# Kernel optimization log

Hardware: AMD Instinct MI355X
Metric: run time of the kernel (lower is better)

Reference implementation:

```python
import jax, jax.numpy as jnp
import numpy as np

# --- model hyperparams (match PointFeatureNet / FastFlow3D SetConvLayer) ---
B, N, IN_CH = 4, 4096, 6
K = 64                      # max_num_neighbors in radius query (PyG FlowNet3D convention)
R1, RATIO1 = 0.5, 0.5       # set_conv_1
R2, RATIO2 = 1.0, 0.25      # set_conv_2
MLP1_DIMS = [IN_CH, 32, 32, 64]        # concat(feat(3), dpos(3)) -> 64
MLP2_DIMS = [64 + 3, 64, 64, 128]      # concat(feat(64), dpos(3)) -> 128


def _mlp_params(key, dims, scale=0.1):
    params = []
    for cin, cout in zip(dims[:-1], dims[1:]):
        key, kw, kb = jax.random.split(key, 3)
        params.append((jax.random.normal(kw, (cin, cout), jnp.float32) * scale,
                       jax.random.normal(kb, (cout,), jnp.float32) * scale))
    return params, key


def setup_inputs() -> dict:
    key = jax.random.key(0)
    key, kx = jax.random.split(key)
    x = jax.random.normal(kx, (B, N, IN_CH), jnp.float32)
    p1, key = _mlp_params(key, MLP1_DIMS)
    p2, key = _mlp_params(key, MLP2_DIMS)
    (w1a, b1a), (w1b, b1b), (w1c, b1c) = p1
    (w2a, b2a), (w2b, b2b), (w2c, b2c) = p2
    return {"x": x,
            "w1a": w1a, "b1a": b1a, "w1b": w1b, "b1b": b1b, "w1c": w1c, "b1c": b1c,
            "w2a": w2a, "b2a": b2a, "w2b": w2b, "b2b": b2b, "w2c": w2c, "b2c": b2c}


def fps(pos, n_samples):
    """Farthest point sampling on one cloud. pos: [N,3] -> idx [n_samples] int32.
    Deterministic start at index 0 (PyG fps uses a random start)."""
    n = pos.shape[0]
    def step(carry, _):
        min_d, last = carry
        d = jnp.sum((pos - pos[last]) ** 2, axis=-1)
        min_d = jnp.minimum(min_d, d)
        nxt = jnp.argmax(min_d).astype(jnp.int32)
        return (min_d, nxt), nxt
    init = (jnp.full((n,), jnp.inf, pos.dtype), jnp.asarray(0, jnp.int32))
    _, idx = jax.lax.scan(step, init, None, length=n_samples - 1)
    return jnp.concatenate([jnp.zeros((1,), jnp.int32), idx])


def ball_query(pos, q_pos, r):
    """Fixed-size radius query: up to K lowest-index points within r of each query.
    pos: [N,3], q_pos: [S,3] -> (idx [S,K] int32, valid [S,K] bool)."""
    n = pos.shape[0]
    d2 = jnp.sum((q_pos[:, None, :] - pos[None, :, :]) ** 2, axis=-1)   # [S,N]
    in_r = d2 <= (r * r)
    # prefer lowest source index among in-radius points (mimics PyG radius ordering)
    score = jnp.where(in_r, -jnp.arange(n, dtype=jnp.float32), -jnp.inf)
    s, idx = jax.lax.top_k(score, K)
    valid = jnp.isfinite(s)
    idx = jnp.where(valid, idx, 0).astype(jnp.int32)
    return idx, valid


def set_conv(feat, pos, r, ratio, params):
    """SetConvLayer: fps -> radius grouping -> PointNetConv(local MLP) -> max-pool.
    feat: [B,N,C], pos: [B,N,3] -> (feat' [B,S,Cout], pos' [B,S,3])."""
    n = pos.shape[1]
    s = int(n * ratio)
    idx = jax.vmap(lambda p: fps(p, s))(pos)                              # [B,S]
    q_pos = jax.vmap(lambda p, i: p[i])(pos, idx)                         # [B,S,3]
    nidx, valid = jax.vmap(lambda p, q: ball_query(p, q, r))(pos, q_pos)  # [B,S,K]
    npos = jax.vmap(lambda p, i: p[i])(pos, nidx)                         # [B,S,K,3]
    nfeat = jax.vmap(lambda f, i: f[i])(feat, nidx)                       # [B,S,K,C]
    # PointNetConv message: concat(x_j, pos_j - pos_i) -> MLP (Linear+ReLU chain)
    h = jnp.concatenate([nfeat, npos - q_pos[:, :, None, :]], axis=-1)    # [B,S,K,C+3]
    for w, b in params:
        h = jax.nn.relu(h @ w + b)
    h = jnp.where(valid[..., None], h, -jnp.inf)
    out = jnp.max(h, axis=2)          # max aggregation over neighborhood
    return out, q_pos


def reference(x, w1a, b1a, w1b, b1b, w1c, b1c, w2a, b2a, w2b, b2b, w2c, b2c):
    pos = x[..., :3]
    feat = x[..., 3:]
    p1 = [(w1a, b1a), (w1b, b1b), (w1c, b1c)]
    p2 = [(w2a, b2a), (w2b, b2b), (w2c, b2c)]
    feat, pos = set_conv(feat, pos, R1, RATIO1, p1)
    feat, pos = set_conv(feat, pos, R2, RATIO2, p2)
    b, s = pos.shape[:2]
    batch = jnp.repeat(jnp.arange(b, dtype=jnp.int32), s)
    return feat.reshape(b * s, -1), pos.reshape(b * s, 3), batch
```

## Files before the change

### kernel.cpp

```cpp
#include <hip/hip_runtime.h>
#include <math.h>

#define DEV __device__ __forceinline__

typedef float v2f __attribute__((ext_vector_type(2)));

DEV float d2_exact(float ax, float ay, float az, float bx, float by, float bz) {
  float dx = __fsub_rn(ax, bx);
  float dy = __fsub_rn(ay, by);
  float dz = __fsub_rn(az, bz);
  return __fadd_rn(__fadd_rn(__fmul_rn(dx, dx), __fmul_rn(dy, dy)),
                   __fmul_rn(dz, dz));
}

DEV float uni(float f) {
  return __int_as_float(__builtin_amdgcn_readfirstlane(__float_as_int(f)));
}

template <int CTRL, int RM>
DEV float dppmax_mv(float v) {
  int s = __builtin_amdgcn_update_dpp((int)0xFF800000u, __float_as_int(v), CTRL,
                                      RM, 0xf, false);
  return __int_as_float(s);
}

DEV float rdlane(float v, int src) {
  return __int_as_float(__builtin_amdgcn_readlane(__float_as_int(v), src));
}

struct __align__(16) FpsPart {
  unsigned long long key[2][4];
  float4 pos[2][4];
};

template <int PPT>
DEV void fps_core(const float* __restrict__ p, int stride, int S,
                  float* __restrict__ q, float* __restrict__ px,
                  float* __restrict__ py, float* __restrict__ pz,
                  int* __restrict__ sel, FpsPart* part) {
#pragma clang fp contract(off)
  constexpr int N = PPT * 256;
  constexpr int NP = PPT / 2;
  const int tid = threadIdx.x;
  const int lane = tid & 63, wv = tid >> 6;
  const int base = tid * PPT;

  for (int n = tid; n < N; n += 256) {
    px[n] = p[(size_t)n * stride + 0];
    py[n] = p[(size_t)n * stride + 1];
    pz[n] = p[(size_t)n * stride + 2];
  }
  if (tid == 0) sel[0] = 0;
  __syncthreads();

  v2f mx2[NP], my2[NP], mz2[NP], md2[NP];
#pragma unroll
  for (int j = 0; j < NP; ++j) {
    int n = base + 2 * j;
    mx2[j] = (v2f){px[n], px[n + 1]};
    my2[j] = (v2f){py[n], py[n + 1]};
    mz2[j] = (v2f){pz[n], pz[n + 1]};
    md2[j] = (v2f){INFINITY, INFINITY};
  }

  float lx = uni(px[0]), ly = uni(py[0]), lz = uni(pz[0]);

  for (int s = 1; s < S; ++s) {
    v2f cx2 = (v2f){lx, lx};
    v2f cy2 = (v2f){ly, ly};
    v2f cz2 = (v2f){lz, lz};
    v2f bmax = (v2f){-INFINITY, -INFINITY};
#pragma unroll
    for (int j = 0; j < NP; ++j) {
      v2f dx = mx2[j] - cx2;
      v2f dy = my2[j] - cy2;
      v2f dz = mz2[j] - cz2;
      v2f xx = dx * dx;
      v2f yy = dy * dy;
      v2f zz = dz * dz;
      v2f ss = (xx + yy) + zz;
      v2f m = __builtin_elementwise_min(md2[j], ss);
      md2[j] = m;
      bmax = __builtin_elementwise_max(bmax, m);
    }
    float bv = fmaxf(bmax.x, bmax.y);

    float m0 = bv;
    m0 = fmaxf(m0, dppmax_mv<0x111, 0xf>(m0));
    m0 = fmaxf(m0, dppmax_mv<0x112, 0xf>(m0));
    m0 = fmaxf(m0, dppmax_mv<0x114, 0xf>(m0));
    m0 = fmaxf(m0, dppmax_mv<0x118, 0xf>(m0));
    m0 = fmaxf(m0, dppmax_mv<0x142, 0xa>(m0));
    m0 = fmaxf(m0, dppmax_mv<0x143, 0xc>(m0));

    int bk = 0;
#pragma unroll
    for (int j = NP - 1; j >= 0; --j) {
      if (md2[j].y == bv) bk = 2 * j + 1;
      if (md2[j].x == bv) bk = 2 * j;
    }
    int bi = base + bk;

    float vmax =
        __int_as_float(__builtin_amdgcn_readlane(__float_as_int(m0), 63));
    unsigned long long mk = __ballot(bv == vmax);
    int src = __ffsll(mk) - 1;
    int wi = __builtin_amdgcn_readlane(bi, src);

    float wx = px[wi], wy = py[wi], wz = pz[wi];

    const int sb = s & 1;
    if (lane == 0) {
      part->key[sb][wv] =
          ((unsigned long long)(unsigned int)__float_as_int(vmax) << 32) |
          (unsigned int)~wi;
      part->pos[sb][wv] = make_float4(wx, wy, wz, 0.f);
    }
    __syncthreads();

    ulonglong2 k01 = *(const ulonglong2*)&part->key[sb][0];
    ulonglong2 k23 = *(const ulonglong2*)&part->key[sb][2];
    float4 p0 = part->pos[sb][0];
    float4 p1 = part->pos[sb][1];
    float4 p2 = part->pos[sb][2];
    float4 p3 = part->pos[sb][3];

    bool c01 = k01.x >= k01.y;
    unsigned long long kA = c01 ? k01.x : k01.y;
    float ax = c01 ? p0.x : p1.x;
    float ay = c01 ? p0.y : p1.y;
    float az = c01 ? p0.z : p1.z;
    bool c23 = k23.x >= k23.y;
    unsigned long long kB = c23 ? k23.x : k23.y;
    float bx = c23 ? p2.x : p3.x;
    float by = c23 ? p2.y : p3.y;
    float bz = c23 ? p2.z : p3.z;
    bool cab = kA >= kB;
    unsigned long long kb = cab ? kA : kB;
    lx = cab ? ax : bx;
    ly = cab ? ay : by;
    lz = cab ? az : bz;

    if (tid == 0) sel[s] = (int)~(unsigned int)kb;
  }

  __syncthreads();
  for (int s = tid; s < S; s += 256) {
    int i = sel[s];
    q[s * 3 + 0] = px[i];
    q[s * 3 + 1] = py[i];
    q[s * 3 + 2] = pz[i];
  }
}

__global__ __launch_bounds__(256) void fps1_kernel(const float* __restrict__ x,
                                                   float* __restrict__ qpos1) {
  __shared__ __align__(16) float smem[4096 * 3 + 48 + 2048];
  const float* p = x + (size_t)blockIdx.x * 4096 * 6;
  float* q = qpos1 + (size_t)blockIdx.x * 2048 * 3;
  fps_core<16>(p, 6, 2048, q, smem, smem + 4096, smem + 8192,
               (int*)(smem + 12288 + 48), (FpsPart*)(smem + 12288));
}

template <int CIN, int COUT, int WSTRIDE>
DEV void mlp_layer(const float* __restrict__ hin, float* __restrict__ hout,
                   const float* __restrict__ w, const float* __restrict__ b) {
#pragma unroll
  for (int j = 0; j < COUT; j += 4) {
    float4 acc = *(const float4*)(b + j);
#pragma unroll
    for (int c = 0; c < CIN; ++c) {
      float4 wvec = *(const float4*)(w + (size_t)c * WSTRIDE + j);
      acc.x = fmaf(hin[c], wvec.x, acc.x);
      acc.y = fmaf(hin[c], wvec.y, acc.y);
      acc.z = fmaf(hin[c], wvec.z, acc.z);
      acc.w = fmaf(hin[c], wvec.w, acc.w);
    }
    hout[j + 0] = fmaxf(acc.x, 0.f);
    hout[j + 1] = fmaxf(acc.y, 0.f);
    hout[j + 2] = fmaxf(acc.z, 0.f);
    hout[j + 3] = fmaxf(acc.w, 0.f);
  }
}

DEV void pool64(float* v, int lane) {
#pragma unroll
  for (int o = 32; o >= 1; o >>= 1) {
    bool bit = (lane & o) != 0;
#pragma unroll
    for (int j = 0; j < o; ++j) {
      float send = bit ? v[j] : v[j + o];
      float keep = bit ? v[j + o] : v[j];
      float recv = __shfl_xor(send, o, 64);
      v[j] = fmaxf(keep, recv);
    }
  }
}

DEV int ball_query_wave(const float* __restrict__ pos, int stride, int n_pts,
                        float qx, float qy, float qz, float r2, int lane,
                        int* __restrict__ nls, bool& valid) {
  int cnt = 0;
  for (int base = 0; base < n_pts && cnt < 64; base += 64) {
    int n = base + lane;
    float d2 = d2_exact(pos[(size_t)n * stride + 0], pos[(size_t)n * stride + 1],
                        pos[(size_t)n * stride + 2], qx, qy, qz);
    bool in = (d2 <= r2);
    unsigned long long m = __ballot(in);
    int slot = cnt + (int)__popcll(m & ((1ull << lane) - 1ull));
    if (in && slot < 64) nls[slot] = n;
    cnt += (int)__popcll(m);
  }
  int kcnt = cnt < 64 ? cnt : 64;
  valid = lane < kcnt;
  return valid ? nls[lane] : 0;
}

__global__ __launch_bounds__(256) void sc1_fps2_kernel(
    const float* __restrict__ x, const float* __restrict__ qpos1,
    const float* __restrict__ wa, const float* __restrict__ ba,
    const float* __restrict__ wb, const float* __restrict__ bb,
    const float* __restrict__ wc, const float* __restrict__ bc,
    float* __restrict__ feat1, float* __restrict__ qpos2) {
  __shared__ __align__(16) float smem[2048 * 3 + 48 + 512];

  if (blockIdx.x < 4) {
    const float* p = qpos1 + (size_t)blockIdx.x * 2048 * 3;
    float* q = qpos2 + (size_t)blockIdx.x * 512 * 3;
    fps_core<8>(p, 3, 512, q, smem, smem + 2048, smem + 4096,
                (int*)(smem + 6144 + 48), (FpsPart*)(smem + 6144));
    return;
  }

  int* nls = (int*)smem;
  const int lane = threadIdx.x & 63, wv = threadIdx.x >> 6;
  const int qi = (blockIdx.x - 4) * 4 + wv;
  const int b = qi >> 11;
  const float* xb = x + (size_t)b * 4096 * 6;
  const float qx = qpos1[qi * 3 + 0], qy = qpos1[qi * 3 + 1],
              qz = qpos1[qi * 3 + 2];

  bool valid;
  int nb =
      ball_query_wave(xb, 6, 4096, qx, qy, qz, 0.25f, lane, nls + wv * 64, valid);

  const float* xr = xb + (size_t)nb * 6;
  float h0[6];
  h0[0] = xr[3];
  h0[1] = xr[4];
  h0[2] = xr[5];
  h0[3] = xr[0] - qx;
  h0[4] = xr[1] - qy;
  h0[5] = xr[2] - qz;

  float h1[32];
  mlp_layer<6, 32, 32>(h0, h1, wa, ba);
  float h2[32];
  mlp_layer<32, 32, 32>(h1, h2, wb, bb);
  float h3[64];
  mlp_layer<32, 64, 64>(h2, h3, wc, bc);

  if (!valid) {
#pragma unroll
    for (int j = 0; j < 64; ++j) h3[j] = -INFINITY;
  }
  pool64(h3, lane);
  feat1[(size_t)qi * 64 + lane] = h3[0];
}

__global__ __launch_bounds__(256) void setconv2_kernel(
    const float* __restrict__ feat1, const float* __restrict__ qpos1,
    const float* __restrict__ qpos2, const float* __restrict__ wa,
    const float* __restrict__ ba, const float* __restrict__ wb,
    const float* __restrict__ bb, const float* __restrict__ wc,
    const float* __restrict__ bc, float* __restrict__ feat_out,
    float* __restrict__ batch) {
  __shared__ int nls[4][64];
  const int lane = threadIdx.x & 63, wv = threadIdx.x >> 6;
  const int qi = blockIdx.x * 4 + wv;
  const int b = qi >> 9;
  const float* pb = qpos1 + (size_t)b * 2048 * 3;
  const float* fb = feat1 + (size_t)b * 2048 * 64;
  const float qx = qpos2[qi * 3 + 0], qy = qpos2[qi * 3 + 1],
              qz = qpos2[qi * 3 + 2];

  if (threadIdx.x < 4) {
    int j = blockIdx.x * 4 + threadIdx.x;
    batch[j] = (float)(j >> 9);
  }

  bool valid;
  int nb = ball_query_wave(pb, 3, 2048, qx, qy, qz, 1.0f, lane, nls[wv], valid);

  float h0[67];
  {
    const float* fr = fb + (size_t)nb * 64;
#pragma unroll
    for (int c = 0; c < 64; c += 4) {
      float4 v = *(const float4*)(fr + c);
      h0[c + 0] = v.x;
      h0[c + 1] = v.y;
      h0[c + 2] = v.z;
      h0[c + 3] = v.w;
    }
    const float* pr = pb + (size_t)nb * 3;
    h0[64] = pr[0] - qx;
    h0[65] = pr[1] - qy;
    h0[66] = pr[2] - qz;
  }

  float h1[64];
  mlp_layer<67, 64, 64>(h0, h1, wa, ba);
  float h2[64];
  mlp_layer<64, 64, 64>(h1, h2, wb, bb);

#pragma unroll 1
  for (int half = 0; half < 2; ++half) {
    float h3[64];
    mlp_layer<64, 64, 128>(h2, h3, wc + half * 64, bc + half * 64);
    if (!valid) {
#pragma unroll
      for (int j = 0; j < 64; ++j) h3[j] = -INFINITY;
    }
    pool64(h3, lane);
    feat_out[(size_t)qi * 128 + half * 64 + lane] = h3[0];
  }
}

extern "C" void kernel_launch(void* const* d_in, const int* in_sizes, int n_in,
                              void* d_out, int out_size, void* d_ws,
                              size_t ws_size, hipStream_t stream) {
  const float* x   = (const float*)d_in[0];
  const float* w1a = (const float*)d_in[1];
  const float* b1a = (const float*)d_in[2];
  const float* w1b = (const float*)d_in[3];
  const float* b1b = (const float*)d_in[4];
  const float* w1c = (const float*)d_in[5];
  const float* b1c = (const float*)d_in[6];
  const float* w2a = (const float*)d_in[7];
  const float* b2a = (const float*)d_in[8];
  const float* w2b = (const float*)d_in[9];
  const float* b2b = (const float*)d_in[10];
  const float* w2c = (const float*)d_in[11];
  const float* b2c = (const float*)d_in[12];

  float* out = (float*)d_out;
  float* qpos1 = (float*)d_ws;
  float* feat1 = qpos1 + 4 * 2048 * 3;
  float* feat2 = out;
  float* qpos2 = out + 2048 * 128;
  float* batch = out + 2048 * 128 + 2048 * 3;

  fps1_kernel<<<4, 256, 0, stream>>>(x, qpos1);
  sc1_fps2_kernel<<<2052, 256, 0, stream>>>(x, qpos1, w1a, b1a, w1b, b1b, w1c,
                                            b1c, feat1, qpos2);
  setconv2_kernel<<<512, 256, 0, stream>>>(feat1, qpos1, qpos2, w2a, b2a, w2b,
                                           b2b, w2c, b2c, feat2, batch);
}
```

Measured before the change: 1.626 ms.

## Run first-level FPS with a single wavefront per cloud to avoid block syncs

Replaces the 256-thread block FPS for the first set conv with a single 64-lane wavefront per cloud. Each lane holds 64 points in registers and picks the argmax with DPP and ballot reductions, so no shared-memory partials or __syncthreads are needed per iteration. In exchange each lane does four times more distance work per step and carries heavy register pressure (256 floats of point state), with only 4 waves on the whole GPU.

```diff
diff --git a/kernel.cpp b/kernel.cpp
--- a/kernel.cpp
+++ b/kernel.cpp
@@ -26,6 +26,92 @@
 
 DEV float rdlane(float v, int src) {
   return __int_as_float(__builtin_amdgcn_readlane(__float_as_int(v), src));
+}
+
+template <int PPT>
+DEV void fps_wave(const float* __restrict__ p, int stride, int S,
+                  float* __restrict__ q, float* __restrict__ px,
+                  float* __restrict__ py, float* __restrict__ pz) {
+#pragma clang fp contract(off)
+  constexpr int N = PPT * 64;
+  constexpr int NP = PPT / 2;
+  const int lane = threadIdx.x & 63;
+  const int base = lane * PPT;
+
+  for (int n = lane; n < N; n += 64) {
+    px[n] = p[(size_t)n * stride + 0];
+    py[n] = p[(size_t)n * stride + 1];
+    pz[n] = p[(size_t)n * stride + 2];
+  }
+
+  v2f mx2[NP], my2[NP], mz2[NP], md2[NP];
+#pragma unroll
+  for (int j = 0; j < NP; ++j) {
+    int n = base + 2 * j;
+    mx2[j] = (v2f){px[n], px[n + 1]};
+    my2[j] = (v2f){py[n], py[n + 1]};
+    mz2[j] = (v2f){pz[n], pz[n + 1]};
+    md2[j] = (v2f){INFINITY, INFINITY};
+  }
+
+  float lx = uni(px[0]), ly = uni(py[0]), lz = uni(pz[0]);
+  if (lane == 0) {
+    q[0] = lx;
+    q[1] = ly;
+    q[2] = lz;
+  }
+
+  for (int s = 1; s < S; ++s) {
+    v2f cx2 = (v2f){lx, lx};
+    v2f cy2 = (v2f){ly, ly};
+    v2f cz2 = (v2f){lz, lz};
+    v2f bmax = (v2f){-INFINITY, -INFINITY};
+#pragma unroll
+    for (int j = 0; j < NP; ++j) {
+      v2f dx = mx2[j] - cx2;
+      v2f dy = my2[j] - cy2;
+      v2f dz = mz2[j] - cz2;
+      v2f xx = dx * dx;
+      v2f yy = dy * dy;
+      v2f zz = dz * dz;
+      v2f ss = (xx + yy) + zz;
+      v2f m = __builtin_elementwise_min(md2[j], ss);
+      md2[j] = m;
+      bmax = __builtin_elementwise_max(bmax, m);
+    }
+    float bv = fmaxf(bmax.x, bmax.y);
+
+    float m0 = bv;
+    m0 = fmaxf(m0, dppmax_mv<0x111, 0xf>(m0));
+    m0 = fmaxf(m0, dppmax_mv<0x112, 0xf>(m0));
+    m0 = fmaxf(m0, dppmax_mv<0x114, 0xf>(m0));
+    m0 = fmaxf(m0, dppmax_mv<0x118, 0xf>(m0));
+    m0 = fmaxf(m0, dppmax_mv<0x142, 0xa>(m0));
+    m0 = fmaxf(m0, dppmax_mv<0x143, 0xc>(m0));
+
+    int bk = 0;
+#pragma unroll
+    for (int j = NP - 1; j >= 0; --j) {
+      if (md2[j].y == bv) bk = 2 * j + 1;
+      if (md2[j].x == bv) bk = 2 * j;
+    }
+    int bi = base + bk;
+
+    float vmax =
+        __int_as_float(__builtin_amdgcn_readlane(__float_as_int(m0), 63));
+    unsigned long long mk = __ballot(bv == vmax);
+    int src = __ffsll(mk) - 1;
+    int wi = __builtin_amdgcn_readlane(bi, src);
+
+    lx = uni(px[wi]);
+    ly = uni(py[wi]);
+    lz = uni(pz[wi]);
+    if (lane == 0) {
+      q[s * 3 + 0] = lx;
+      q[s * 3 + 1] = ly;
+      q[s * 3 + 2] = lz;
+    }
+  }
 }
 
 struct __align__(16) FpsPart {
@@ -153,13 +239,12 @@
   }
 }
 
-__global__ __launch_bounds__(256) void fps1_kernel(const float* __restrict__ x,
-                                                   float* __restrict__ qpos1) {
-  __shared__ __align__(16) float smem[4096 * 3 + 48 + 2048];
+__global__ __launch_bounds__(64) void fps1_kernel(const float* __restrict__ x,
+                                                  float* __restrict__ qpos1) {
+  __shared__ __align__(16) float smem[4096 * 3];
   const float* p = x + (size_t)blockIdx.x * 4096 * 6;
   float* q = qpos1 + (size_t)blockIdx.x * 2048 * 3;
-  fps_core<16>(p, 6, 2048, q, smem, smem + 4096, smem + 8192,
-               (int*)(smem + 12288 + 48), (FpsPart*)(smem + 12288));
+  fps_wave<64>(p, 6, 2048, q, smem, smem + 4096, smem + 8192);
 }
 
 template <int CIN, int COUT, int WSTRIDE>
@@ -351,7 +436,7 @@
   float* qpos2 = out + 2048 * 128;
   float* batch = out + 2048 * 128 + 2048 * 3;
 
-  fps1_kernel<<<4, 256, 0, stream>>>(x, qpos1);
+  fps1_kernel<<<4, 64, 0, stream>>>(x, qpos1);
   sc1_fps2_kernel<<<2052, 256, 0, stream>>>(x, qpos1, w1a, b1a, w1b, b1b, w1c,
                                             b1c, feat1, qpos2);
   setconv2_kernel<<<512, 256, 0, stream>>>(feat1, qpos1, qpos2, w2a, b2a, w2b,
```

New measurement: 3.449 ms. +112.1%, slower.
